# Performance work log

Measured on AMD Instinct MI355X. Metric: run time of the kernel, lower is better.

Reference implementation:

```python
import jax, jax.numpy as jnp
import numpy as np

TEMP = 0.05            # self.temp
NUM_INSTANCES = 16     # self.num_instances


def _l2norm(x):
    return x / jnp.linalg.norm(x, axis=-1, keepdims=True)


def setup_inputs() -> dict:
    key = jax.random.key(0)
    ks = jax.random.split(key, 6)
    B, D, N, K, NDATA = 256, 2048, 32768, 8192, 100000
    inputs = jax.random.normal(ks[0], (B, D), jnp.float32)
    # memory bank rows are kept unit-norm by the momentum update; init normalized
    features = _l2norm(jax.random.normal(ks[1], (N, D), jnp.float32))
    kmeans_centeroids = jax.random.normal(ks[2], (K, D), jnp.float32)
    targets = jax.random.randint(ks[3], (B,), 0, N)
    kmeans_pids = jax.random.randint(ks[4], (NDATA,), 0, K)
    indexes = jax.random.randint(ks[5], (B,), 0, NDATA)
    return {"inputs": inputs, "features": features,
            "kmeans_centeroids": kmeans_centeroids, "targets": targets,
            "kmeans_pids": kmeans_pids, "indexes": indexes, "neg_size": 20}


def reference(inputs, features, kmeans_centeroids, targets, kmeans_pids,
              indexes, neg_size):
    B = inputs.shape[0]
    K = kmeans_centeroids.shape[0]
    x = _l2norm(inputs)                                   # F.normalize(inputs, dim=1)
    outputs = x @ features.T                              # CM.forward: [B, N]
    finch_pos = jnp.take_along_axis(outputs, targets[:, None], axis=1)  # [B,1]
    kmeans_score = x @ kmeans_centeroids.T                # [B, K]
    batch_kmeans_pids = kmeans_pids[indexes]              # [B]
    # scatter_(-2) own kmeans cluster, then take top-neg_size negatives
    masked = jax.lax.stop_gradient(kmeans_score)          # detach().clone()
    masked = masked.at[jnp.arange(B), batch_kmeans_pids].set(-2.0)
    _, sel_ind_neg = jax.lax.top_k(masked, neg_size)      # [B, neg_size]
    kmeans_chosen_neg = jnp.take_along_axis(kmeans_score, sel_ind_neg, axis=1)
    mixed_score = jnp.concatenate([finch_pos, kmeans_chosen_neg], axis=1) / TEMP
    # confidence mask: per group of NUM_INSTANCES (first half of batch),
    # sample agrees with the group's modal kmeans pid (np.bincount().argmax())
    half = B // 2
    g = batch_kmeans_pids[:half].reshape(-1, NUM_INSTANCES)        # [G, I]
    counts = jax.nn.one_hot(g, K, dtype=jnp.int32).sum(axis=1)     # [G, K]
    mode = jnp.argmax(counts, axis=1)                              # ties -> smallest id
    mask_half = (g == mode[:, None]).reshape(-1).astype(jnp.float32)
    confidence_mask = jnp.concatenate([mask_half, mask_half])      # [B]
    # CE(mixed_score, 0) per-sample, confidence-weighted mean
    ce_neg = -jax.nn.log_softmax(mixed_score, axis=1)[:, 0]
    neg_con_loss = (confidence_mask * ce_neg).mean()
    # CE(outputs/temp, targets) mean
    logp = jax.nn.log_softmax(outputs / TEMP, axis=1)
    ce_main = -jnp.take_along_axis(logp, targets[:, None], axis=1).mean()
    return 0.2 * neg_con_loss + ce_main
```

## Files before the change

### kernel.cpp

```cpp
#include <hip/hip_runtime.h>
#include <stdint.h>

typedef __attribute__((ext_vector_type(8))) short short8;
typedef __attribute__((ext_vector_type(4))) float floatx4;

__device__ __forceinline__ unsigned short f2b(float f) {
    union { float f; uint32_t u; } v; v.f = f;
    uint32_t u = v.u;
    return (unsigned short)((u + 0x7FFFu + ((u >> 16) & 1u)) >> 16);
}

__device__ __forceinline__ uint32_t pk2(float a, float b) {
    union { float f; uint32_t u; } x, y; x.f = a; y.f = b;
    uint32_t ua = x.u + 0x8000u, ub = y.u + 0x8000u;
    return (ua >> 16) | (ub & 0xFFFF0000u);
}

__device__ __forceinline__ void async16(const void* g, void* l) {
    __builtin_amdgcn_global_load_lds(
        (const __attribute__((address_space(1))) void*)g,
        (__attribute__((address_space(3))) void*)l, 16, 0, 0);
}

__global__ void norm_kernel(const float* __restrict__ in,
                            unsigned short* __restrict__ xb, int D) {
    int b = blockIdx.x, t = threadIdx.x;
    const float* row = in + (size_t)b * D;
    float ss = 0.f;
    for (int i = t * 4; i < D; i += 1024) {
        float4 v = *(const float4*)(row + i);
        ss += v.x * v.x + v.y * v.y + v.z * v.z + v.w * v.w;
    }
    for (int off = 32; off > 0; off >>= 1) ss += __shfl_down(ss, off);
    __shared__ float wsum[4];
    __shared__ float rn_sh;
    if ((t & 63) == 0) wsum[t >> 6] = ss;
    __syncthreads();
    if (t == 0) rn_sh = rsqrtf(wsum[0] + wsum[1] + wsum[2] + wsum[3]);
    __syncthreads();
    float rn = rn_sh;
    unsigned short* orow = xb + (size_t)b * D;
    for (int i = t * 4; i < D; i += 1024) {
        float4 v = *(const float4*)(row + i);
        ushort4 o;
        o.x = f2b(v.x * rn); o.y = f2b(v.y * rn);
        o.z = f2b(v.z * rn); o.w = f2b(v.w * rn);
        *(ushort4*)(orow + i) = o;
    }
}

#define BKk 64
__global__ __launch_bounds__(256, 2)
void gemm_kernel(const unsigned short* __restrict__ xb,
                 const float* __restrict__ featB,
                 const float* __restrict__ centB,
                 const int* __restrict__ targets,
                 float* __restrict__ S, float* __restrict__ pos,
                 float* __restrict__ km,
                 int D, int K, int nbF) {
    __shared__ __align__(16) unsigned short Alds[2][256 * BKk];
    __shared__ __align__(16) unsigned short Blds[2][64 * BKk];

    const int t = threadIdx.x;
    const int w = t >> 6, l = t & 63;
    const bool isFeat = ((int)blockIdx.x < nbF);
    const int n0 = (isFeat ? (int)blockIdx.x : ((int)blockIdx.x - nbF)) * 64;
    const float* Bsrc = isFeat ? featB : centB;

    floatx4 acc[4][4];
#pragma unroll
    for (int ti = 0; ti < 4; ++ti)
#pragma unroll
        for (int tj = 0; tj < 4; ++tj)
            acc[ti][tj] = (floatx4){0.f, 0.f, 0.f, 0.f};

    const int kIters = D / BKk;
    const int brow = t >> 2, bq = t & 3;
    const float* bg0 = Bsrc + (size_t)(n0 + brow) * D + bq * 16;
    const int bc0 = ((bq * 2) ^ (brow & 7)) * 16;
    const int bc1 = ((bq * 2 + 1) ^ (brow & 7)) * 16;
    const char* xbB = (const char*)xb;

    auto stageA = [&](int nb, int ktn) {
#pragma unroll
        for (int j = 0; j < 8; ++j) {
            int slin = j * 256 + t;
            int r = slin >> 3;
            int cg = (slin & 7) ^ (r & 7);
            async16(xbB + (size_t)r * (D * 2) + (size_t)ktn * (BKk * 2) + cg * 16,
                    (char*)(&Alds[nb][0]) + slin * 16);
        }
    };

    auto compute = [&](int cb) {
        const char* Ab = (const char*)(&Alds[cb][0]);
        const char* Bb = (const char*)(&Blds[cb][0]);
#pragma unroll
        for (int s = 0; s < 2; ++s) {
            short8 aF[4], bF[4];
#pragma unroll
            for (int ti = 0; ti < 4; ++ti) {
                int R = w * 64 + ti * 16 + (l & 15);
                int g = s * 4 + (l >> 4);
                aF[ti] = *(const short8*)(Ab + R * 128 + ((g ^ (R & 7)) * 16));
            }
#pragma unroll
            for (int tj = 0; tj < 4; ++tj) {
                int Rn = tj * 16 + (l & 15);
                int g = s * 4 + (l >> 4);
                bF[tj] = *(const short8*)(Bb + Rn * 128 + ((g ^ (Rn & 7)) * 16));
            }
#pragma unroll
            for (int ti = 0; ti < 4; ++ti)
#pragma unroll
                for (int tj = 0; tj < 4; ++tj)
                    acc[ti][tj] = __builtin_amdgcn_mfma_f32_16x16x32_bf16(
                        aF[ti], bF[tj], acc[ti][tj], 0, 0, 0);
        }
    };

    stageA(0, 0);
    {
        const float* bg = bg0;
        float4 f0 = *(const float4*)(bg);
        float4 f1 = *(const float4*)(bg + 4);
        float4 f2 = *(const float4*)(bg + 8);
        float4 f3 = *(const float4*)(bg + 12);
        uint4 p0, p1;
        p0.x = pk2(f0.x, f0.y); p0.y = pk2(f0.z, f0.w);
        p0.z = pk2(f1.x, f1.y); p0.w = pk2(f1.z, f1.w);
        p1.x = pk2(f2.x, f2.y); p1.y = pk2(f2.z, f2.w);
        p1.z = pk2(f3.x, f3.y); p1.w = pk2(f3.z, f3.w);
        char* bb = (char*)(&Blds[0][0]) + brow * 128;
        *(uint4*)(bb + bc0) = p0;
        *(uint4*)(bb + bc1) = p1;
    }
    __syncthreads();

    for (int kt = 0; kt < kIters - 1; ++kt) {
        const int cb = kt & 1, nb = cb ^ 1;
        stageA(nb, kt + 1);
        const float* bg = bg0 + (kt + 1) * BKk;
        float4 f0 = *(const float4*)(bg);
        float4 f1 = *(const float4*)(bg + 4);
        float4 f2 = *(const float4*)(bg + 8);
        float4 f3 = *(const float4*)(bg + 12);

        compute(cb);

        uint4 p0, p1;
        p0.x = pk2(f0.x, f0.y); p0.y = pk2(f0.z, f0.w);
        p0.z = pk2(f1.x, f1.y); p0.w = pk2(f1.z, f1.w);
        p1.x = pk2(f2.x, f2.y); p1.y = pk2(f2.z, f2.w);
        p1.z = pk2(f3.x, f3.y); p1.w = pk2(f3.z, f3.w);
        char* bb = (char*)(&Blds[nb][0]) + brow * 128;
        *(uint4*)(bb + bc0) = p0;
        *(uint4*)(bb + bc1) = p1;
        __syncthreads();
    }
    compute((kIters - 1) & 1);

    if (isFeat) {
#pragma unroll
        for (int ti = 0; ti < 4; ++ti) {
#pragma unroll
            for (int r = 0; r < 4; ++r) {
                int row = w * 64 + ti * 16 + ((l >> 4) << 2) + r;
                int tr = targets[row];
                int col0 = n0 + (l & 15);
                float e = 0.f;
#pragma unroll
                for (int tj = 0; tj < 4; ++tj) {
                    float c = acc[ti][tj][r];
                    e += __expf(c * 20.0f);
                    if (tr == col0 + tj * 16) pos[row] = c;
                }
                e += __shfl_xor(e, 1); e += __shfl_xor(e, 2);
                e += __shfl_xor(e, 4); e += __shfl_xor(e, 8);
                if ((l & 15) == 0) atomicAdd(&S[row], e);
            }
        }
    } else {
#pragma unroll
        for (int ti = 0; ti < 4; ++ti) {
#pragma unroll
            for (int r = 0; r < 4; ++r) {
                int row = w * 64 + ti * 16 + ((l >> 4) << 2) + r;
                size_t base = (size_t)row * K + n0 + (l & 15);
#pragma unroll
                for (int tj = 0; tj < 4; ++tj)
                    km[base + tj * 16] = acc[ti][tj][r];
            }
        }
    }
}

__global__ __launch_bounds__(256, 4)
void topk_kernel(const float* __restrict__ kmr,
                 const int* __restrict__ pids,
                 const int* __restrict__ idxs,
                 const int* __restrict__ negsz,
                 float* __restrict__ topv, int K) {
    int b = blockIdx.x, t = threadIdx.x;
    int w = t >> 6, l = t & 63;
    const float* row = kmr + (size_t)b * K;
    float v[32];
#pragma unroll
    for (int k = 0; k < 32; ++k) v[k] = row[k * 256 + t];
    int gi = pids[idxs[b]];
    if ((gi & 255) == t) {
        int kk = gi >> 8;
#pragma unroll
        for (int k = 0; k < 32; ++k) if (k == kk) v[k] = -1e30f;
    }
    float bv = v[0]; int bk = 0;
#pragma unroll
    for (int k = 1; k < 32; ++k) if (v[k] > bv) { bv = v[k]; bk = k; }

    __shared__ float rv[4];
    __shared__ int rg[4];
    int ns = *negsz; if (ns > 32) ns = 32;
    for (int j = 0; j < ns; ++j) {
        float mv = bv; int mg = bk * 256 + t;
#pragma unroll
        for (int off = 1; off < 64; off <<= 1) {
            float ov = __shfl_xor(mv, off);
            int og = __shfl_xor(mg, off);
            if (ov > mv) { mv = ov; mg = og; }
        }
        if (l == 0) { rv[w] = mv; rg[w] = mg; }
        __syncthreads();
        float gv = rv[0]; int gg = rg[0];
#pragma unroll
        for (int ww = 1; ww < 4; ++ww)
            if (rv[ww] > gv) { gv = rv[ww]; gg = rg[ww]; }
        if (t == 0) topv[b * 32 + j] = gv;
        if ((gg & 255) == t) {
            int kk = gg >> 8;
#pragma unroll
            for (int k = 0; k < 32; ++k) if (k == kk) v[k] = -1e30f;
            bv = v[0]; bk = 0;
#pragma unroll
            for (int k = 1; k < 32; ++k) if (v[k] > bv) { bv = v[k]; bk = k; }
        }
        __syncthreads();
    }
}

__global__ void final_kernel(const float* __restrict__ S,
                             const float* __restrict__ pos,
                             const float* __restrict__ topv,
                             const int* __restrict__ pids,
                             const int* __restrict__ idxs,
                             const int* __restrict__ negsz,
                             float* __restrict__ out, int B) {
    __shared__ int pid_sh[256];
    __shared__ int mode_sh[16];
    __shared__ float red[256];
    int t = threadIdx.x;
    if (t < B) pid_sh[t] = pids[idxs[t]];
    __syncthreads();
    int half = B >> 1;
    int G = half / 16;
    if (t < G) {
        int bestPid = 0x7FFFFFFF, bestCnt = -1;
        for (int i = 0; i < 16; ++i) {
            int p = pid_sh[t * 16 + i];
            int c = 0;
            for (int j = 0; j < 16; ++j) c += (pid_sh[t * 16 + j] == p) ? 1 : 0;
            if (c > bestCnt || (c == bestCnt && p < bestPid)) { bestCnt = c; bestPid = p; }
        }
        mode_sh[t] = bestPid;
    }
    __syncthreads();
    float contrib = 0.f;
    if (t < B) {
        int hb = (t < half) ? t : t - half;
        float mask = (pid_sh[hb] == mode_sh[hb / 16]) ? 1.f : 0.f;
        int ns = *negsz; if (ns > 32) ns = 32;
        float p20 = pos[t] * 20.0f;
        float m = p20;
        for (int j = 0; j < ns; ++j) m = fmaxf(m, topv[t * 32 + j] * 20.0f);
        float se = __expf(p20 - m);
        for (int j = 0; j < ns; ++j) se += __expf(topv[t * 32 + j] * 20.0f - m);
        float ce_neg = m + logf(se) - p20;
        float ce_main = logf(S[t]) - p20;
        contrib = (0.2f * mask * ce_neg + ce_main) / (float)B;
    }
    red[t] = contrib;
    __syncthreads();
    for (int s = 128; s > 0; s >>= 1) {
        if (t < s) red[t] += red[t + s];
        __syncthreads();
    }
    if (t == 0) out[0] = red[0];
}

extern "C" void kernel_launch(void* const* d_in, const int* in_sizes, int n_in,
                              void* d_out, int out_size, void* d_ws, size_t ws_size,
                              hipStream_t stream) {
    const float* inputs   = (const float*)d_in[0];
    const float* features = (const float*)d_in[1];
    const float* cents    = (const float*)d_in[2];
    const int*   targets  = (const int*)d_in[3];
    const int*   pids     = (const int*)d_in[4];
    const int*   idxs     = (const int*)d_in[5];
    const int*   negsz    = (const int*)d_in[6];
    float* out = (float*)d_out;

    int Bb = in_sizes[3];
    int Dd = in_sizes[0] / Bb;
    int Nn = in_sizes[1] / Dd;
    int Kk = in_sizes[2] / Dd;

    char* ws = (char*)d_ws;
    unsigned short* xb = (unsigned short*)ws;
    size_t o = (size_t)Bb * Dd * 2;
    float* km   = (float*)(ws + o); o += (size_t)Bb * Kk * 4;
    float* S    = (float*)(ws + o); o += (size_t)Bb * 4;
    float* pos  = (float*)(ws + o); o += (size_t)Bb * 4;
    float* topv = (float*)(ws + o); o += (size_t)Bb * 32 * 4;

    hipMemsetAsync(S, 0, (size_t)Bb * 4, stream);
    norm_kernel<<<Bb, 256, 0, stream>>>(inputs, xb, Dd);
    int nbF = Nn / 64, nbC = Kk / 64;
    gemm_kernel<<<nbF + nbC, 256, 0, stream>>>(xb, features, cents, targets,
                                               S, pos, km, Dd, Kk, nbF);
    topk_kernel<<<Bb, 256, 0, stream>>>(km, pids, idxs, negsz, topv, Kk);
    final_kernel<<<1, 256, 0, stream>>>(S, pos, topv, pids, idxs, negsz, out, Bb);
}
```

Before: 549.7 us.

## Restructure GEMM main loop with register prefetch of B and explicit waitcnt barriers

Reorganizes the K loop so the fp32 B tile for the next iteration is loaded into registers a full iteration ahead, while the current tile is packed to bf16 and written to LDS before compute. It replaces __syncthreads with explicit s_waitcnt vmcnt/lgkmcnt and raw s_barrier so the async A loads and the B global loads can remain in flight across compute. This adds register pressure from the extra float4 buffers and depends on the hand-counted vmcnt(12) matching the number of outstanding loads. Two barriers per iteration are used instead of one.

```diff
diff --git a/kernel.cpp b/kernel.cpp
--- a/kernel.cpp
+++ b/kernel.cpp
@@ -119,46 +119,40 @@
         }
     };
 
+    float4 f0, f1, f2, f3, g0, g1, g2, g3;
     stageA(0, 0);
-    {
-        const float* bg = bg0;
-        float4 f0 = *(const float4*)(bg);
-        float4 f1 = *(const float4*)(bg + 4);
-        float4 f2 = *(const float4*)(bg + 8);
-        float4 f3 = *(const float4*)(bg + 12);
+    f0 = *(const float4*)(bg0);
+    f1 = *(const float4*)(bg0 + 4);
+    f2 = *(const float4*)(bg0 + 8);
+    f3 = *(const float4*)(bg0 + 12);
+
+    for (int kt = 0; kt < kIters; ++kt) {
+        const int cb = kt & 1, nb = cb ^ 1;
+        if (kt + 1 < kIters) {
+            stageA(nb, kt + 1);
+            const float* bg = bg0 + (kt + 1) * BKk;
+            g0 = *(const float4*)(bg);
+            g1 = *(const float4*)(bg + 4);
+            g2 = *(const float4*)(bg + 8);
+            g3 = *(const float4*)(bg + 12);
+            asm volatile("s_waitcnt vmcnt(12)" ::: "memory");
+        } else {
+            asm volatile("s_waitcnt vmcnt(0)" ::: "memory");
+        }
         uint4 p0, p1;
         p0.x = pk2(f0.x, f0.y); p0.y = pk2(f0.z, f0.w);
         p0.z = pk2(f1.x, f1.y); p0.w = pk2(f1.z, f1.w);
         p1.x = pk2(f2.x, f2.y); p1.y = pk2(f2.z, f2.w);
         p1.z = pk2(f3.x, f3.y); p1.w = pk2(f3.z, f3.w);
-        char* bb = (char*)(&Blds[0][0]) + brow * 128;
+        char* bb = (char*)(&Blds[cb][0]) + brow * 128;
         *(uint4*)(bb + bc0) = p0;
         *(uint4*)(bb + bc1) = p1;
-    }
-    __syncthreads();
-
-    for (int kt = 0; kt < kIters - 1; ++kt) {
-        const int cb = kt & 1, nb = cb ^ 1;
-        stageA(nb, kt + 1);
-        const float* bg = bg0 + (kt + 1) * BKk;
-        float4 f0 = *(const float4*)(bg);
-        float4 f1 = *(const float4*)(bg + 4);
-        float4 f2 = *(const float4*)(bg + 8);
-        float4 f3 = *(const float4*)(bg + 12);
-
+        asm volatile("s_waitcnt lgkmcnt(0)" ::: "memory");
+        __builtin_amdgcn_s_barrier();
         compute(cb);
-
-        uint4 p0, p1;
-        p0.x = pk2(f0.x, f0.y); p0.y = pk2(f0.z, f0.w);
-        p0.z = pk2(f1.x, f1.y); p0.w = pk2(f1.z, f1.w);
-        p1.x = pk2(f2.x, f2.y); p1.y = pk2(f2.z, f2.w);
-        p1.z = pk2(f3.x, f3.y); p1.w = pk2(f3.z, f3.w);
-        char* bb = (char*)(&Blds[nb][0]) + brow * 128;
-        *(uint4*)(bb + bc0) = p0;
-        *(uint4*)(bb + bc1) = p1;
-        __syncthreads();
-    }
-    compute((kIters - 1) & 1);
+        __builtin_amdgcn_s_barrier();
+        f0 = g0; f1 = g1; f2 = g2; f3 = g3;
+    }
 
     if (isFeat) {
 #pragma unroll
```

Result: no change. 551.8 us (+0.4%).
